# Kernel tuning notes

Measured on AMD Instinct MI355X. Metric: run time of the kernel, lower is better.

Reference implementation:

```python
import jax, jax.numpy as jnp
import numpy as np

IN_DIM, ATT_DIM, OUT_DIM, NH = 1024, 64, 64, 16
ATT_BIAS = 0.5


def setup_inputs() -> dict:
    key = jax.random.key(0)
    ks = jax.random.split(key, 11)
    B, S = 2, 2048
    s_in = 1.0 / np.sqrt(IN_DIM)
    s_o = 1.0 / np.sqrt(NH * OUT_DIM)
    return {
        "q": jax.random.normal(ks[0], (B, S, IN_DIM), jnp.float32),
        "k": jax.random.normal(ks[1], (B, S, IN_DIM), jnp.float32),
        "v": jax.random.normal(ks[2], (B, S, IN_DIM), jnp.float32),
        "Wq": jax.random.uniform(ks[3], (IN_DIM, NH * ATT_DIM), jnp.float32, -s_in, s_in),
        "bq": jax.random.uniform(ks[4], (NH * ATT_DIM,), jnp.float32, -s_in, s_in),
        "Wk": jax.random.uniform(ks[5], (IN_DIM, NH * ATT_DIM), jnp.float32, -s_in, s_in),
        "bk": jax.random.uniform(ks[6], (NH * ATT_DIM,), jnp.float32, -s_in, s_in),
        "Wv": jax.random.uniform(ks[7], (IN_DIM, NH * OUT_DIM), jnp.float32, -s_in, s_in),
        "bv": jax.random.uniform(ks[8], (NH * OUT_DIM,), jnp.float32, -s_in, s_in),
        "Wo": jax.random.uniform(ks[9], (NH * OUT_DIM, OUT_DIM), jnp.float32, -s_o, s_o),
        "bo": jax.random.uniform(ks[10], (OUT_DIM,), jnp.float32, -s_o, s_o),
    }


def reference(q, k, v, Wq, bq, Wk, bk, Wv, bv, Wo, bo):
    B, S, _ = q.shape
    scale = ATT_DIM ** -0.5
    # projections -> [B, H, S, d]
    qh = (q @ Wq + bq).reshape(B, S, NH, ATT_DIM).transpose(0, 2, 1, 3)
    kh = (k @ Wk + bk).reshape(B, S, NH, ATT_DIM).transpose(0, 2, 1, 3)
    vh = (v @ Wv + bv).reshape(B, S, NH, OUT_DIM).transpose(0, 2, 1, 3)
    # sigmoid-biased scores then softmax over keys
    scores = jnp.einsum("bhqd,bhkd->bhqk", qh * scale, kh)
    scores = jax.nn.sigmoid(scores) - ATT_BIAS
    attn = jax.nn.softmax(scores, axis=-1)
    out = jnp.einsum("bhqk,bhkd->bhqd", attn, vh)  # dropout p=0 -> identity
    out = out.transpose(0, 2, 1, 3).reshape(B, S, NH * OUT_DIM)
    return out @ Wo + bo
```

## Files before the change

kernel.cpp:

```cpp
#include <hip/hip_runtime.h>
#include <hip/hip_bf16.h>
#include <stdint.h>

typedef __bf16 bf16x8 __attribute__((ext_vector_type(8)));
typedef float  f32x4  __attribute__((ext_vector_type(4)));

__device__ __forceinline__ unsigned short f2bf(float f) {
  union { float f; unsigned u; } x; x.f = f;
  unsigned r = x.u + 0x7fffu + ((x.u >> 16) & 1u);
  return (unsigned short)(r >> 16);
}

__device__ __forceinline__ unsigned pack_rne(float a, float b) {
  unsigned ua = __float_as_uint(a), ub = __float_as_uint(b);
  ua = ua + 0x7fffu + ((ua >> 16) & 1u);
  ub = ub + 0x7fffu + ((ub >> 16) & 1u);
  return __builtin_amdgcn_perm(ub, ua, 0x07060302);
}

__device__ __forceinline__ void gll16(const void* g, void* l) {
  __builtin_amdgcn_global_load_lds((const __attribute__((address_space(1))) void*)g,
                                   (__attribute__((address_space(3))) void*)l, 16, 0, 0);
}

__device__ __forceinline__ void stage64(unsigned short* dst, const unsigned short* src,
                                        int rowstride, int w, int lane) {
  #pragma unroll
  for (int i = 0; i < 2; ++i) {
    int cc = i * 256 + w * 64 + lane;
    int r = cc >> 3;
    int j = (cc & 7) ^ (r & 7);
    gll16(src + (size_t)r * rowstride + j * 8, dst + (size_t)(i * 256 + w * 64) * 8);
  }
}

__global__ __launch_bounds__(256) void k_convert(
    const float* __restrict__ q, const float* __restrict__ k, const float* __restrict__ v,
    unsigned short* __restrict__ qb, unsigned short* __restrict__ kb, unsigned short* __restrict__ vb) {
  const float* src = blockIdx.z == 0 ? q : blockIdx.z == 1 ? k : v;
  unsigned short* dst = blockIdx.z == 0 ? qb : blockIdx.z == 1 ? kb : vb;
  size_t i = (size_t)blockIdx.x * 256 + threadIdx.x;
  float4 f = ((const float4*)src)[i];
  ushort4 o;
  o.x = f2bf(f.x); o.y = f2bf(f.y); o.z = f2bf(f.z); o.w = f2bf(f.w);
  ((ushort4*)dst)[i] = o;
}

__global__ __launch_bounds__(256) void k_transpose(
    const float* __restrict__ Wq, const float* __restrict__ Wk,
    const float* __restrict__ Wv, const float* __restrict__ Wo,
    unsigned short* __restrict__ Wqt, unsigned short* __restrict__ Wkt,
    unsigned short* __restrict__ Wvt, unsigned short* __restrict__ Wot) {
  int z = blockIdx.z;
  const float* W = z == 0 ? Wq : z == 1 ? Wk : z == 2 ? Wv : Wo;
  unsigned short* Wt = z == 0 ? Wqt : z == 1 ? Wkt : z == 2 ? Wvt : Wot;
  int C = (z < 3) ? 1024 : 64;
  int c0 = blockIdx.x * 32, r0 = blockIdx.y * 32;
  if (c0 >= C) return;
  __shared__ float t[32][33];
  int tx = threadIdx.x, ty = threadIdx.y;
  #pragma unroll
  for (int i = 0; i < 32; i += 8)
    t[ty + i][tx] = W[(size_t)(r0 + ty + i) * C + c0 + tx];
  __syncthreads();
  #pragma unroll
  for (int i = 0; i < 32; i += 8)
    Wt[(size_t)(c0 + ty + i) * 1024 + r0 + tx] = f2bf(t[tx][ty + i]);
}

__global__ __launch_bounds__(256) void k_proj(
    const unsigned short* __restrict__ qb, const unsigned short* __restrict__ kb,
    const unsigned short* __restrict__ vb,
    const unsigned short* __restrict__ Wqt, const unsigned short* __restrict__ Wkt,
    const unsigned short* __restrict__ Wvt,
    const float* __restrict__ bq, const float* __restrict__ bk, const float* __restrict__ bv,
    unsigned short* __restrict__ qh, unsigned short* __restrict__ kh,
    unsigned short* __restrict__ vht) {
  int z = blockIdx.z;
  const unsigned short* A  = z == 0 ? qb  : z == 1 ? kb  : vb;
  const unsigned short* Bt = z == 0 ? Wqt : z == 1 ? Wkt : Wvt;
  const float* bias = z == 0 ? bq : z == 1 ? bk : bv;

  int m0 = blockIdx.y * 128;
  int n0 = blockIdx.x * 128;

  __shared__ __attribute__((aligned(16))) unsigned short As[128 * 32];
  __shared__ __attribute__((aligned(16))) unsigned short Bs[128 * 32];

  int tid = threadIdx.x;
  int w = tid >> 6, lane = tid & 63;
  int wm = w >> 1, wn = w & 1;
  int lr = lane & 15, lk = lane >> 4;

  f32x4 acc[4][4] = {};

  for (int k0 = 0; k0 < 1024; k0 += 32) {
    #pragma unroll
    for (int i = 0; i < 2; ++i) {
      int c = i * 256 + w * 64 + lane;
      int r = c >> 2;
      int kb_ = (c & 3) ^ ((r >> 1) & 3);
      gll16(A + (size_t)(m0 + r) * 1024 + k0 + kb_ * 8, As + (size_t)(i * 256 + w * 64) * 8);
    }
    #pragma unroll
    for (int i = 0; i < 2; ++i) {
      int c = i * 256 + w * 64 + lane;
      int r = c >> 2;
      int kb_ = (c & 3) ^ ((r >> 1) & 3);
      gll16(Bt + (size_t)(n0 + r) * 1024 + k0 + kb_ * 8, Bs + (size_t)(i * 256 + w * 64) * 8);
    }
    __syncthreads();
    bf16x8 af[4], bfr[4];
    #pragma unroll
    for (int mt = 0; mt < 4; ++mt) {
      int r = wm * 64 + mt * 16 + lr;
      int ch = r * 4 + (lk ^ ((r >> 1) & 3));
      af[mt] = *(const bf16x8*)(As + ch * 8);
    }
    #pragma unroll
    for (int nt = 0; nt < 4; ++nt) {
      int r = wn * 64 + nt * 16 + lr;
      int ch = r * 4 + (lk ^ ((r >> 1) & 3));
      bfr[nt] = *(const bf16x8*)(Bs + ch * 8);
    }
    #pragma unroll
    for (int mt = 0; mt < 4; ++mt)
      #pragma unroll
      for (int nt = 0; nt < 4; ++nt)
        acc[mt][nt] = __builtin_amdgcn_mfma_f32_16x16x32_bf16(af[mt], bfr[nt], acc[mt][nt], 0, 0, 0);
    __syncthreads();
  }

  #pragma unroll
  for (int nt = 0; nt < 4; ++nt) {
    int n = n0 + wn * 64 + nt * 16 + lr;
    float bv_ = bias[n];
    int h = n >> 6, d = n & 63;
    #pragma unroll
    for (int mt = 0; mt < 4; ++mt) {
      int mbase = m0 + wm * 64 + mt * 16 + lk * 4;
      int b = mbase >> 11, s = mbase & 2047;
      if (z == 2) {
        size_t o = ((size_t)(b * 16 + h) * 64 + d) * 2048 + s;
        ushort4 pk;
        pk.x = f2bf(acc[mt][nt][0] + bv_);
        pk.y = f2bf(acc[mt][nt][1] + bv_);
        pk.z = f2bf(acc[mt][nt][2] + bv_);
        pk.w = f2bf(acc[mt][nt][3] + bv_);
        *(ushort4*)(vht + o) = pk;
      } else {
        unsigned short* dst = (z == 0) ? qh : kh;
        float sc = (z == 0) ? 0.125f : 1.0f;
        #pragma unroll
        for (int rg = 0; rg < 4; ++rg) {
          float val = (acc[mt][nt][rg] + bv_) * sc;
          float pv = __shfl_xor(val, 1, 64);
          if ((lr & 1) == 0) {
            unsigned pkv = pack_rne(val, pv);
            *(unsigned*)(dst + ((size_t)(b * 16 + h) * 2048 + (s + rg)) * 64 + d) = pkv;
          }
        }
      }
    }
  }
}

__global__ __launch_bounds__(256, 4) void k_attn(
    const unsigned short* __restrict__ qh, const unsigned short* __restrict__ kh,
    const unsigned short* __restrict__ vht, unsigned short* __restrict__ attout) {
  int bh = blockIdx.y;
  int q0 = blockIdx.x * 64;
  const unsigned short* Q = qh + (size_t)bh * 2048 * 64;
  const unsigned short* K = kh + (size_t)bh * 2048 * 64;
  const unsigned short* V = vht + (size_t)bh * 64 * 2048;

  __shared__ __attribute__((aligned(16))) unsigned short KV[16384];
  __shared__ float lsum[64];

  int tid = threadIdx.x;
  int w = tid >> 6, lane = tid & 63;
  int wm = w >> 1, wn = w & 1;
  int c = lane & 15, qd = lane >> 4;

  bf16x8 qf[2][2];
  #pragma unroll
  for (int nt = 0; nt < 2; ++nt)
    #pragma unroll
    for (int ks = 0; ks < 2; ++ks)
      qf[nt][ks] = *(const bf16x8*)(Q + (size_t)(q0 + wn * 32 + nt * 16 + c) * 64 + ks * 32 + qd * 8);

  stage64(KV, K, 64, w, lane);
  stage64(KV + 4096, V, 2048, w, lane);
  __syncthreads();

  f32x4 o[4][2] = {};
  float qs[2] = {0.f, 0.f};

  for (int kt = 0; kt < 32; ++kt) {
    int cur = kt & 1;
    unsigned short* Kc = KV + cur * 8192;
    unsigned short* Vc = Kc + 4096;
    if (kt + 1 < 32) {
      unsigned short* Kn = KV + (cur ^ 1) * 8192;
      stage64(Kn, K + (size_t)(kt + 1) * 4096, 64, w, lane);
      stage64(Kn + 4096, V + (size_t)(kt + 1) * 64, 2048, w, lane);
    }

    f32x4 s[2][2] = {};
    #pragma unroll
    for (int ks = 0; ks < 2; ++ks) {
      bf16x8 kf[2];
      #pragma unroll
      for (int mt = 0; mt < 2; ++mt) {
        int r = wm * 32 + mt * 16 + c;
        int ch = r * 8 + ((ks * 4 + qd) ^ (r & 7));
        kf[mt] = *(const bf16x8*)(Kc + ch * 8);
      }
      #pragma unroll
      for (int mt = 0; mt < 2; ++mt)
        #pragma unroll
        for (int nt = 0; nt < 2; ++nt)
          s[mt][nt] = __builtin_amdgcn_mfma_f32_16x16x32_bf16(kf[mt], qf[nt][ks], s[mt][nt], 0, 0, 0);
    }

    unsigned pk[2][2][2];
    #pragma unroll
    for (int mt = 0; mt < 2; ++mt)
      #pragma unroll
      for (int nt = 0; nt < 2; ++nt) {
        unsigned wu[4];
        #pragma unroll
        for (int rg = 0; rg < 4; ++rg) {
          float t = __expf(s[mt][nt][rg]);
          float u = __builtin_amdgcn_rcpf(1.0f + t);
          float e = __expf(-u);
          unsigned eu = __float_as_uint(e) & 0xffff0000u;
          qs[nt] += __uint_as_float(eu);
          wu[rg] = eu;
        }
        pk[mt][nt][0] = __builtin_amdgcn_perm(wu[1], wu[0], 0x07060302);
        pk[mt][nt][1] = __builtin_amdgcn_perm(wu[3], wu[2], 0x07060302);
      }

    bf16x8 vf[4];
    #pragma unroll
    for (int dt = 0; dt < 4; ++dt) {
      int r = dt * 16 + c;
      int ch = r * 8 + ((wm * 4 + qd) ^ (r & 7));
      vf[dt] = *(const bf16x8*)(Vc + ch * 8);
    }
    #pragma unroll
    for (int nt = 0; nt < 2; ++nt) {
      union { unsigned u[4]; bf16x8 v; } bfr;
      #pragma unroll
      for (int d = 0; d < 4; ++d) {
        int srcl = (((2 * qd + (d >> 1)) & 3) << 4) | c;
        unsigned lo = (unsigned)__shfl((int)pk[0][nt][d & 1], srcl, 64);
        unsigned hi = (unsigned)__shfl((int)pk[1][nt][d & 1], srcl, 64);
        bfr.u[d] = (lane >= 32) ? hi : lo;
      }
      #pragma unroll
      for (int dt = 0; dt < 4; ++dt)
        o[dt][nt] = __builtin_amdgcn_mfma_f32_16x16x32_bf16(vf[dt], bfr.v, o[dt][nt], 0, 0, 0);
    }
    __syncthreads();
  }

  #pragma unroll
  for (int nt = 0; nt < 2; ++nt) {
    qs[nt] += __shfl_xor(qs[nt], 16, 64);
    qs[nt] += __shfl_xor(qs[nt], 32, 64);
  }

  float* Ored = (float*)KV;
  if (wm == 1) {
    #pragma unroll
    for (int nt = 0; nt < 2; ++nt) {
      int ql = wn * 32 + nt * 16 + c;
      #pragma unroll
      for (int dt = 0; dt < 4; ++dt)
        *(f32x4*)(Ored + ql * 64 + dt * 16 + qd * 4) = o[dt][nt];
      if (qd == 0) lsum[ql] = qs[nt];
    }
  }
  __syncthreads();
  if (wm == 0) {
    int b = bh >> 4, h = bh & 15;
    #pragma unroll
    for (int nt = 0; nt < 2; ++nt) {
      int ql = wn * 32 + nt * 16 + c;
      float inv = __builtin_amdgcn_rcpf(qs[nt] + lsum[ql]);
      size_t rowoff = ((size_t)(b * 2048 + q0 + ql)) * 1024 + h * 64;
      #pragma unroll
      for (int dt = 0; dt < 4; ++dt) {
        f32x4 r = *(const f32x4*)(Ored + ql * 64 + dt * 16 + qd * 4);
        f32x4 t = o[dt][nt];
        uint2 pko;
        pko.x = pack_rne((t[0] + r[0]) * inv, (t[1] + r[1]) * inv);
        pko.y = pack_rne((t[2] + r[2]) * inv, (t[3] + r[3]) * inv);
        *(uint2*)(attout + rowoff + dt * 16 + qd * 4) = pko;
      }
    }
  }
}

__global__ __launch_bounds__(256) void k_oinit(const float* __restrict__ bo,
                                               float* __restrict__ out) {
  int i = blockIdx.x * 256 + threadIdx.x;
  out[i] = bo[i & 63];
}

__global__ __launch_bounds__(256) void k_oproj(
    const unsigned short* __restrict__ attout, const unsigned short* __restrict__ Wot,
    float* __restrict__ out) {
  int m0 = blockIdx.x * 64;
  int kbase = blockIdx.y * 256;
  __shared__ __attribute__((aligned(16))) unsigned short As[64 * 32];
  __shared__ __attribute__((aligned(16))) unsigned short Bs[64 * 32];
  int tid = threadIdx.x;
  int w = tid >> 6, lane = tid & 63;
  int lr = lane & 15, lk = lane >> 4;

  f32x4 acc[4] = {};

  for (int k0 = kbase; k0 < kbase + 256; k0 += 32) {
    {
      int c = tid;
      int r = c >> 2;
      int kb_ = (c & 3) ^ ((r >> 1) & 3);
      gll16(attout + (size_t)(m0 + r) * 1024 + k0 + kb_ * 8, As + (size_t)(w * 64) * 8);
      gll16(Wot + (size_t)r * 1024 + k0 + kb_ * 8, Bs + (size_t)(w * 64) * 8);
    }
    __syncthreads();
    bf16x8 af, bfr[4];
    {
      int r = w * 16 + lr;
      int ch = r * 4 + (lk ^ ((r >> 1) & 3));
      af = *(const bf16x8*)(As + ch * 8);
    }
    #pragma unroll
    for (int nt = 0; nt < 4; ++nt) {
      int r = nt * 16 + lr;
      int ch = r * 4 + (lk ^ ((r >> 1) & 3));
      bfr[nt] = *(const bf16x8*)(Bs + ch * 8);
    }
    #pragma unroll
    for (int nt = 0; nt < 4; ++nt)
      acc[nt] = __builtin_amdgcn_mfma_f32_16x16x32_bf16(af, bfr[nt], acc[nt], 0, 0, 0);
    __syncthreads();
  }
  #pragma unroll
  for (int nt = 0; nt < 4; ++nt) {
    int n = nt * 16 + lr;
    #pragma unroll
    for (int rg = 0; rg < 4; ++rg) {
      int m = m0 + w * 16 + lk * 4 + rg;
      atomicAdd(&out[(size_t)m * 64 + n], acc[nt][rg]);
    }
  }
}

extern "C" void kernel_launch(void* const* d_in, const int* in_sizes, int n_in,
                              void* d_out, int out_size, void* d_ws, size_t ws_size,
                              hipStream_t stream) {
  const float* q  = (const float*)d_in[0];
  const float* k  = (const float*)d_in[1];
  const float* v  = (const float*)d_in[2];
  const float* Wq = (const float*)d_in[3];
  const float* bq = (const float*)d_in[4];
  const float* Wk = (const float*)d_in[5];
  const float* bk = (const float*)d_in[6];
  const float* Wv = (const float*)d_in[7];
  const float* bv = (const float*)d_in[8];
  const float* Wo = (const float*)d_in[9];
  const float* bo = (const float*)d_in[10];
  float* out = (float*)d_out;

  char* ws = (char*)d_ws;
  const size_t MB = 1024 * 1024;
  unsigned short* qb  = (unsigned short*)(ws + 0 * MB);
  unsigned short* kb  = (unsigned short*)(ws + 8 * MB);
  unsigned short* vb  = (unsigned short*)(ws + 16 * MB);
  unsigned short* Wqt = (unsigned short*)(ws + 24 * MB);
  unsigned short* Wkt = (unsigned short*)(ws + 26 * MB);
  unsigned short* Wvt = (unsigned short*)(ws + 28 * MB);
  unsigned short* Wot = (unsigned short*)(ws + 30 * MB);
  unsigned short* qh  = (unsigned short*)(ws + 32 * MB);
  unsigned short* kh  = (unsigned short*)(ws + 40 * MB);
  unsigned short* vht = (unsigned short*)(ws + 48 * MB);
  unsigned short* att = (unsigned short*)(ws + 56 * MB);

  k_convert<<<dim3(4096, 1, 3), dim3(256), 0, stream>>>(q, k, v, qb, kb, vb);
  k_transpose<<<dim3(32, 32, 4), dim3(32, 8), 0, stream>>>(Wq, Wk, Wv, Wo, Wqt, Wkt, Wvt, Wot);
  k_proj<<<dim3(8, 32, 3), dim3(256), 0, stream>>>(qb, kb, vb, Wqt, Wkt, Wvt, bq, bk, bv, qh, kh, vht);
  k_attn<<<dim3(32, 32), dim3(256), 0, stream>>>(qh, kh, vht, att);
  k_oinit<<<dim3(1024), dim3(256), 0, stream>>>(bo, out);
  k_oproj<<<dim3(64, 4), dim3(256), 0, stream>>>(att, Wot, out);
}
```

Measured before the change: 253.4 us.

## Merge prep kernels, deepen proj K-tile, avoid shuffles in attention PV matmul

Fuses the convert, weight-transpose and output-bias-init kernels into one launch, cutting the kernel count from six to four. The projection GEMM now stages a K-slice of 64 per iteration with a wider XOR swizzle, halving the number of barriers, and drops to an occupancy hint of 3. In attention, the PV product uses 16x16x16 MFMAs that take the softmax probabilities directly from registers instead of cross-lane shuffles, and the staging and fragment addresses are precomputed outside the loop. The trade-offs are twice as many MFMA instructions in the PV step, and a fallback inline-asm path with padding nops if the builtin is unavailable.

```diff
diff --git a/kernel.cpp b/kernel.cpp
--- a/kernel.cpp
+++ b/kernel.cpp
@@ -4,6 +4,7 @@
 
 typedef __bf16 bf16x8 __attribute__((ext_vector_type(8)));
 typedef float  f32x4  __attribute__((ext_vector_type(4)));
+typedef short  short4v __attribute__((ext_vector_type(4)));
 
 __device__ __forceinline__ unsigned short f2bf(float f) {
   union { float f; unsigned u; } x; x.f = f;
@@ -18,57 +19,74 @@
   return __builtin_amdgcn_perm(ub, ua, 0x07060302);
 }
 
+__device__ __forceinline__ f32x4 mfma16(short4v a, short4v b, f32x4 c) {
+#if __has_builtin(__builtin_amdgcn_mfma_f32_16x16x16bf16_1k)
+  return __builtin_amdgcn_mfma_f32_16x16x16bf16_1k(a, b, c, 0, 0, 0);
+#else
+  f32x4 d;
+  asm volatile("v_mfma_f32_16x16x16_bf16 %0, %1, %2, %3\n\ts_nop 7\n\ts_nop 7"
+               : "=v"(d) : "v"(a), "v"(b), "v"(c));
+  return d;
+#endif
+}
+
 __device__ __forceinline__ void gll16(const void* g, void* l) {
   __builtin_amdgcn_global_load_lds((const __attribute__((address_space(1))) void*)g,
                                    (__attribute__((address_space(3))) void*)l, 16, 0, 0);
 }
 
-__device__ __forceinline__ void stage64(unsigned short* dst, const unsigned short* src,
-                                        int rowstride, int w, int lane) {
-  #pragma unroll
-  for (int i = 0; i < 2; ++i) {
-    int cc = i * 256 + w * 64 + lane;
-    int r = cc >> 3;
-    int j = (cc & 7) ^ (r & 7);
-    gll16(src + (size_t)r * rowstride + j * 8, dst + (size_t)(i * 256 + w * 64) * 8);
-  }
-}
-
-__global__ __launch_bounds__(256) void k_convert(
+__global__ __launch_bounds__(256) void k_prep(
     const float* __restrict__ q, const float* __restrict__ k, const float* __restrict__ v,
-    unsigned short* __restrict__ qb, unsigned short* __restrict__ kb, unsigned short* __restrict__ vb) {
-  const float* src = blockIdx.z == 0 ? q : blockIdx.z == 1 ? k : v;
-  unsigned short* dst = blockIdx.z == 0 ? qb : blockIdx.z == 1 ? kb : vb;
-  size_t i = (size_t)blockIdx.x * 256 + threadIdx.x;
-  float4 f = ((const float4*)src)[i];
-  ushort4 o;
-  o.x = f2bf(f.x); o.y = f2bf(f.y); o.z = f2bf(f.z); o.w = f2bf(f.w);
-  ((ushort4*)dst)[i] = o;
-}
-
-__global__ __launch_bounds__(256) void k_transpose(
     const float* __restrict__ Wq, const float* __restrict__ Wk,
     const float* __restrict__ Wv, const float* __restrict__ Wo,
+    const float* __restrict__ bo,
+    unsigned short* __restrict__ qb, unsigned short* __restrict__ kb,
+    unsigned short* __restrict__ vb,
     unsigned short* __restrict__ Wqt, unsigned short* __restrict__ Wkt,
-    unsigned short* __restrict__ Wvt, unsigned short* __restrict__ Wot) {
-  int z = blockIdx.z;
-  const float* W = z == 0 ? Wq : z == 1 ? Wk : z == 2 ? Wv : Wo;
-  unsigned short* Wt = z == 0 ? Wqt : z == 1 ? Wkt : z == 2 ? Wvt : Wot;
-  int C = (z < 3) ? 1024 : 64;
-  int c0 = blockIdx.x * 32, r0 = blockIdx.y * 32;
-  if (c0 >= C) return;
-  __shared__ float t[32][33];
-  int tx = threadIdx.x, ty = threadIdx.y;
-  #pragma unroll
-  for (int i = 0; i < 32; i += 8)
-    t[ty + i][tx] = W[(size_t)(r0 + ty + i) * C + c0 + tx];
-  __syncthreads();
-  #pragma unroll
-  for (int i = 0; i < 32; i += 8)
-    Wt[(size_t)(c0 + ty + i) * 1024 + r0 + tx] = f2bf(t[tx][ty + i]);
-}
-
-__global__ __launch_bounds__(256) void k_proj(
+    unsigned short* __restrict__ Wvt, unsigned short* __restrict__ Wot,
+    float* __restrict__ out) {
+  __shared__ float tt[32][33];
+  int b = blockIdx.x, tid = threadIdx.x;
+  if (b < 12288) {
+    int z = b >> 12;
+    const float* src = z == 0 ? q : z == 1 ? k : v;
+    unsigned short* dst = z == 0 ? qb : z == 1 ? kb : vb;
+    size_t i = (size_t)(b & 4095) * 256 + tid;
+    float4 f = ((const float4*)src)[i];
+    ushort4 o;
+    o.x = f2bf(f.x); o.y = f2bf(f.y); o.z = f2bf(f.z); o.w = f2bf(f.w);
+    ((ushort4*)dst)[i] = o;
+  } else if (b < 15424) {
+    int t = b - 12288;
+    const float* W; unsigned short* Wt; int C, c0, r0;
+    if (t < 3072) {
+      int z = t >> 10;
+      W = z == 0 ? Wq : z == 1 ? Wk : Wv;
+      Wt = z == 0 ? Wqt : z == 1 ? Wkt : Wvt;
+      C = 1024; int tile = t & 1023;
+      c0 = (tile & 31) * 32; r0 = (tile >> 5) * 32;
+    } else {
+      int t2 = t - 3072;
+      W = Wo; Wt = Wot; C = 64;
+      c0 = (t2 & 1) * 32; r0 = (t2 >> 1) * 32;
+    }
+    int tx = tid & 31, ty = tid >> 5;
+    #pragma unroll
+    for (int i = 0; i < 32; i += 8)
+      tt[ty + i][tx] = W[(size_t)(r0 + ty + i) * C + c0 + tx];
+    __syncthreads();
+    #pragma unroll
+    for (int i = 0; i < 32; i += 8)
+      Wt[(size_t)(c0 + ty + i) * 1024 + r0 + tx] = f2bf(tt[tx][ty + i]);
+  } else {
+    int t3 = b - 15424;
+    int i = t3 * 1024 + tid * 4;
+    float4 bv4 = *(const float4*)(bo + (i & 63));
+    *(float4*)(out + i) = bv4;
+  }
+}
+
+__global__ __launch_bounds__(256, 3) void k_proj(
     const unsigned short* __restrict__ qb, const unsigned short* __restrict__ kb,
     const unsigned short* __restrict__ vb,
     const unsigned short* __restrict__ Wqt, const unsigned short* __restrict__ Wkt,
@@ -84,8 +102,8 @@
   int m0 = blockIdx.y * 128;
   int n0 = blockIdx.x * 128;
 
-  __shared__ __attribute__((aligned(16))) unsigned short As[128 * 32];
-  __shared__ __attribute__((aligned(16))) unsigned short Bs[128 * 32];
+  __shared__ __attribute__((aligned(16))) unsigned short As[128 * 64];
+  __shared__ __attribute__((aligned(16))) unsigned short Bs[128 * 64];
 
   int tid = threadIdx.x;
   int w = tid >> 6, lane = tid & 63;
@@ -94,40 +112,41 @@
 
   f32x4 acc[4][4] = {};
 
-  for (int k0 = 0; k0 < 1024; k0 += 32) {
-    #pragma unroll
-    for (int i = 0; i < 2; ++i) {
-      int c = i * 256 + w * 64 + lane;
-      int r = c >> 2;
-      int kb_ = (c & 3) ^ ((r >> 1) & 3);
-      gll16(A + (size_t)(m0 + r) * 1024 + k0 + kb_ * 8, As + (size_t)(i * 256 + w * 64) * 8);
-    }
-    #pragma unroll
-    for (int i = 0; i < 2; ++i) {
-      int c = i * 256 + w * 64 + lane;
-      int r = c >> 2;
-      int kb_ = (c & 3) ^ ((r >> 1) & 3);
-      gll16(Bt + (size_t)(n0 + r) * 1024 + k0 + kb_ * 8, Bs + (size_t)(i * 256 + w * 64) * 8);
-    }
-    __syncthreads();
-    bf16x8 af[4], bfr[4];
-    #pragma unroll
-    for (int mt = 0; mt < 4; ++mt) {
-      int r = wm * 64 + mt * 16 + lr;
-      int ch = r * 4 + (lk ^ ((r >> 1) & 3));
-      af[mt] = *(const bf16x8*)(As + ch * 8);
-    }
-    #pragma unroll
-    for (int nt = 0; nt < 4; ++nt) {
-      int r = wn * 64 + nt * 16 + lr;
-      int ch = r * 4 + (lk ^ ((r >> 1) & 3));
-      bfr[nt] = *(const bf16x8*)(Bs + ch * 8);
-    }
-    #pragma unroll
-    for (int mt = 0; mt < 4; ++mt)
-      #pragma unroll
-      for (int nt = 0; nt < 4; ++nt)
-        acc[mt][nt] = __builtin_amdgcn_mfma_f32_16x16x32_bf16(af[mt], bfr[nt], acc[mt][nt], 0, 0, 0);
+  for (int k0 = 0; k0 < 1024; k0 += 64) {
+    #pragma unroll
+    for (int i = 0; i < 4; ++i) {
+      int cc = i * 256 + tid;
+      int r = cc >> 3;
+      int j = (cc & 7) ^ (r & 7);
+      gll16(A + (size_t)(m0 + r) * 1024 + k0 + j * 8, As + (size_t)(i * 256 + w * 64) * 8);
+    }
+    #pragma unroll
+    for (int i = 0; i < 4; ++i) {
+      int cc = i * 256 + tid;
+      int r = cc >> 3;
+      int j = (cc & 7) ^ (r & 7);
+      gll16(Bt + (size_t)(n0 + r) * 1024 + k0 + j * 8, Bs + (size_t)(i * 256 + w * 64) * 8);
+    }
+    __syncthreads();
+    #pragma unroll
+    for (int ks = 0; ks < 2; ++ks) {
+      bf16x8 af[4], bfr[4];
+      #pragma unroll
+      for (int mt = 0; mt < 4; ++mt) {
+        int r = wm * 64 + mt * 16 + lr;
+        af[mt] = *(const bf16x8*)(As + r * 64 + ((ks * 4 + lk) ^ (r & 7)) * 8);
+      }
+      #pragma unroll
+      for (int nt = 0; nt < 4; ++nt) {
+        int r = wn * 64 + nt * 16 + lr;
+        bfr[nt] = *(const bf16x8*)(Bs + r * 64 + ((ks * 4 + lk) ^ (r & 7)) * 8);
+      }
+      #pragma unroll
+      for (int mt = 0; mt < 4; ++mt)
+        #pragma unroll
+        for (int nt = 0; nt < 4; ++nt)
+          acc[mt][nt] = __builtin_amdgcn_mfma_f32_16x16x32_bf16(af[mt], bfr[nt], acc[mt][nt], 0, 0, 0);
+    }
     __syncthreads();
   }
 
@@ -171,8 +190,8 @@
   int bh = blockIdx.y;
   int q0 = blockIdx.x * 64;
   const unsigned short* Q = qh + (size_t)bh * 2048 * 64;
-  const unsigned short* K = kh + (size_t)bh * 2048 * 64;
-  const unsigned short* V = vht + (size_t)bh * 64 * 2048;
+  const unsigned short* Kg = kh + (size_t)bh * 2048 * 64;
+  const unsigned short* Vg = vht + (size_t)bh * 64 * 2048;
 
   __shared__ __attribute__((aligned(16))) unsigned short KV[16384];
   __shared__ float lsum[64];
@@ -189,21 +208,56 @@
     for (int ks = 0; ks < 2; ++ks)
       qf[nt][ks] = *(const bf16x8*)(Q + (size_t)(q0 + wn * 32 + nt * 16 + c) * 64 + ks * 32 + qd * 8);
 
-  stage64(KV, K, 64, w, lane);
-  stage64(KV + 4096, V, 2048, w, lane);
+  size_t kOff[2], vOff[2]; int lOff[2];
+  #pragma unroll
+  for (int i = 0; i < 2; ++i) {
+    int cc = i * 256 + w * 64 + lane;
+    int r = cc >> 3;
+    int j = (cc & 7) ^ (r & 7);
+    kOff[i] = (size_t)r * 64 + j * 8;
+    vOff[i] = (size_t)r * 2048 + j * 8;
+    lOff[i] = (i * 256 + w * 64) * 8;
+  }
+
+  #pragma unroll
+  for (int i = 0; i < 2; ++i) {
+    gll16(Kg + kOff[i], KV + lOff[i]);
+    gll16(Vg + vOff[i], KV + 4096 + lOff[i]);
+  }
+  Kg += 4096; Vg += 64;
+
+  int kfA[2][2], vfA[4][2];
+  #pragma unroll
+  for (int mt = 0; mt < 2; ++mt) {
+    int r = wm * 32 + mt * 16 + c;
+    #pragma unroll
+    for (int ks = 0; ks < 2; ++ks)
+      kfA[mt][ks] = r * 64 + ((ks * 4 + qd) ^ (r & 7)) * 8;
+  }
+  #pragma unroll
+  for (int dt = 0; dt < 4; ++dt) {
+    int r = dt * 16 + c;
+    #pragma unroll
+    for (int mt = 0; mt < 2; ++mt)
+      vfA[dt][mt] = r * 64 + ((4 * wm + 2 * mt + (qd >> 1)) ^ (r & 7)) * 8 + (qd & 1) * 4;
+  }
+
   __syncthreads();
 
   f32x4 o[4][2] = {};
   float qs[2] = {0.f, 0.f};
 
   for (int kt = 0; kt < 32; ++kt) {
-    int cur = kt & 1;
-    unsigned short* Kc = KV + cur * 8192;
+    unsigned short* Kc = KV + (kt & 1) * 8192;
     unsigned short* Vc = Kc + 4096;
     if (kt + 1 < 32) {
-      unsigned short* Kn = KV + (cur ^ 1) * 8192;
-      stage64(Kn, K + (size_t)(kt + 1) * 4096, 64, w, lane);
-      stage64(Kn + 4096, V + (size_t)(kt + 1) * 64, 2048, w, lane);
+      unsigned short* Kn = KV + ((kt & 1) ^ 1) * 8192;
+      #pragma unroll
+      for (int i = 0; i < 2; ++i) {
+        gll16(Kg + kOff[i], Kn + lOff[i]);
+        gll16(Vg + vOff[i], Kn + 4096 + lOff[i]);
+      }
+      Kg += 4096; Vg += 64;
     }
 
     f32x4 s[2][2] = {};
@@ -211,11 +265,8 @@
     for (int ks = 0; ks < 2; ++ks) {
       bf16x8 kf[2];
       #pragma unroll
-      for (int mt = 0; mt < 2; ++mt) {
-        int r = wm * 32 + mt * 16 + c;
-        int ch = r * 8 + ((ks * 4 + qd) ^ (r & 7));
-        kf[mt] = *(const bf16x8*)(Kc + ch * 8);
-      }
+      for (int mt = 0; mt < 2; ++mt)
+        kf[mt] = *(const bf16x8*)(Kc + kfA[mt][ks]);
       #pragma unroll
       for (int mt = 0; mt < 2; ++mt)
         #pragma unroll
@@ -242,27 +293,23 @@
         pk[mt][nt][1] = __builtin_amdgcn_perm(wu[3], wu[2], 0x07060302);
       }
 
-    bf16x8 vf[4];
-    #pragma unroll
-    for (int dt = 0; dt < 4; ++dt) {
-      int r = dt * 16 + c;
-      int ch = r * 8 + ((wm * 4 + qd) ^ (r & 7));
-      vf[dt] = *(const bf16x8*)(Vc + ch * 8);
-    }
-    #pragma unroll
-    for (int nt = 0; nt < 2; ++nt) {
-      union { unsigned u[4]; bf16x8 v; } bfr;
-      #pragma unroll
-      for (int d = 0; d < 4; ++d) {
-        int srcl = (((2 * qd + (d >> 1)) & 3) << 4) | c;
-        unsigned lo = (unsigned)__shfl((int)pk[0][nt][d & 1], srcl, 64);
-        unsigned hi = (unsigned)__shfl((int)pk[1][nt][d & 1], srcl, 64);
-        bfr.u[d] = (lane >= 32) ? hi : lo;
-      }
-      #pragma unroll
-      for (int dt = 0; dt < 4; ++dt)
-        o[dt][nt] = __builtin_amdgcn_mfma_f32_16x16x32_bf16(vf[dt], bfr.v, o[dt][nt], 0, 0, 0);
-    }
+    short4v vfr[4][2];
+    #pragma unroll
+    for (int dt = 0; dt < 4; ++dt)
+      #pragma unroll
+      for (int mt = 0; mt < 2; ++mt)
+        vfr[dt][mt] = *(const short4v*)(Vc + vfA[dt][mt]);
+    #pragma unroll
+    for (int nt = 0; nt < 2; ++nt)
+      #pragma unroll
+      for (int mt = 0; mt < 2; ++mt) {
+        union { unsigned u[2]; short4v s4; } bb;
+        bb.u[0] = pk[mt][nt][0];
+        bb.u[1] = pk[mt][nt][1];
+        #pragma unroll
+        for (int dt = 0; dt < 4; ++dt)
+          o[dt][nt] = mfma16(vfr[dt][mt], bb.s4, o[dt][nt]);
+      }
     __syncthreads();
   }
 
@@ -302,12 +349,6 @@
       }
     }
   }
-}
-
-__global__ __launch_bounds__(256) void k_oinit(const float* __restrict__ bo,
-                                               float* __restrict__ out) {
-  int i = blockIdx.x * 256 + threadIdx.x;
-  out[i] = bo[i & 63];
 }
 
 __global__ __launch_bounds__(256) void k_oproj(
@@ -325,24 +366,22 @@
 
   for (int k0 = kbase; k0 < kbase + 256; k0 += 32) {
     {
-      int c = tid;
-      int r = c >> 2;
-      int kb_ = (c & 3) ^ ((r >> 1) & 3);
-      gll16(attout + (size_t)(m0 + r) * 1024 + k0 + kb_ * 8, As + (size_t)(w * 64) * 8);
-      gll16(Wot + (size_t)r * 1024 + k0 + kb_ * 8, Bs + (size_t)(w * 64) * 8);
+      int cc = tid;
+      int r = cc >> 2;
+      int j = (cc & 3) ^ ((r >> 1) & 3);
+      gll16(attout + (size_t)(m0 + r) * 1024 + k0 + j * 8, As + (size_t)(w * 64) * 8);
+      gll16(Wot + (size_t)r * 1024 + k0 + j * 8, Bs + (size_t)(w * 64) * 8);
     }
     __syncthreads();
     bf16x8 af, bfr[4];
     {
       int r = w * 16 + lr;
-      int ch = r * 4 + (lk ^ ((r >> 1) & 3));
-      af = *(const bf16x8*)(As + ch * 8);
+      af = *(const bf16x8*)(As + r * 32 + ((lk ^ ((r >> 1) & 3))) * 8);
     }
     #pragma unroll
     for (int nt = 0; nt < 4; ++nt) {
       int r = nt * 16 + lr;
-      int ch = r * 4 + (lk ^ ((r >> 1) & 3));
-      bfr[nt] = *(const bf16x8*)(Bs + ch * 8);
+      bfr[nt] = *(const bf16x8*)(Bs + r * 32 + ((lk ^ ((r >> 1) & 3))) * 8);
     }
     #pragma unroll
     for (int nt = 0; nt < 4; ++nt)
@@ -390,10 +429,10 @@
   unsigned short* vht = (unsigned short*)(ws + 48 * MB);
   unsigned short* att = (unsigned short*)(ws + 56 * MB);
 
-  k_convert<<<dim3(4096, 1, 3), dim3(256), 0, stream>>>(q, k, v, qb, kb, vb);
-  k_transpose<<<dim3(32, 32, 4), dim3(32, 8), 0, stream>>>(Wq, Wk, Wv, Wo, Wqt, Wkt, Wvt, Wot);
-  k_proj<<<dim3(8, 32, 3), dim3(256), 0, stream>>>(qb, kb, vb, Wqt, Wkt, Wvt, bq, bk, bv, qh, kh, vht);
+  k_prep<<<dim3(15680), dim3(256), 0, stream>>>(q, k, v, Wq, Wk, Wv, Wo, bo,
+                                                qb, kb, vb, Wqt, Wkt, Wvt, Wot, out);
+  k_proj<<<dim3(8, 32, 3), dim3(256), 0, stream>>>(qb, kb, vb, Wqt, Wkt, Wvt,
+                                                   bq, bk, bv, qh, kh, vht);
   k_attn<<<dim3(32, 32), dim3(256), 0, stream>>>(qh, kh, vht, att);
-  k_oinit<<<dim3(1024), dim3(256), 0, stream>>>(bo, out);
   k_oproj<<<dim3(64, 4), dim3(256), 0, stream>>>(att, Wot, out);
 }
```

After: 230.2 us. 1.1x faster.
